# Performance work log

Measured on AMD Instinct MI355X. Metric: run time of the kernel, lower is better.

## Reference

```python
import jax, jax.numpy as jnp
from jax import lax
import numpy as np

SIGMA = 0.05  # perturbation std (module default)


def setup_inputs() -> dict:
    key = jax.random.key(0)
    k1, k2, k3 = jax.random.split(key, 3)
    return {
        "scores": jax.random.normal(k1, (8, 32, 32), dtype=jnp.float32),      # scorer output (b, h_score, w_score)
        "x_high": jax.random.normal(k2, (8, 3, 1024, 1024), dtype=jnp.float32),
        "noise": jax.random.normal(k3, (8, 500, 1024), dtype=jnp.float32),    # (b, num_samples, d)
        "k": 16,
        "patch_size": 64,
    }


def reference(scores, x_high, noise, k, patch_size):
    b, hs, ws = scores.shape
    _, c, H, W = x_high.shape
    d = hs * ws
    n = noise.shape[1]
    p = patch_size

    # --- min-max normalize scores (as in DPS.forward) ---
    s = scores.reshape(b, d)
    smin = s.min(axis=-1, keepdims=True)
    smax = s.max(axis=-1, keepdims=True)
    s = (s - smin) / (smax - smin + 1e-5)

    # --- PerturbedTopK forward: mean of one-hot top-k over noise samples ---
    perturbed = s[:, None, :] + noise * SIGMA            # (b, n, d)
    _, idx = lax.top_k(perturbed, k)                     # (b, n, k)
    idx = jnp.sort(idx, axis=-1)
    bi = jnp.arange(b)[:, None, None]
    ki = jnp.arange(k)[None, None, :]
    # scatter-count == one_hot(idx, d).mean(axis=1) without materializing (b,n,k,d)
    indicators = jnp.zeros((b, k, d), s.dtype).at[bi, ki, idx].add(1.0 / n)
    indicators = indicators.reshape(b, k, hs, ws)

    # --- pad high-res image exactly like DPS.__init__ ---
    sh, sw = H // hs, W // ws                            # scale_h, scale_w
    top = (p - sh) // 2
    left = (p - sw) // 2
    padded_h = sh * hs + p - 1
    padded_w = sw * ws + p - 1
    x_pad = jnp.pad(x_high, ((0, 0), (0, 0), (top, padded_h - top - H), (left, padded_w - left - W)))
    # only the first (hs-1)*sh + p rows/cols are ever sliced by the loop
    Eh = (hs - 1) * sh + p
    Ew = (ws - 1) * sw + p
    x_pad = x_pad[:, :, :Eh, :Ew]

    # --- weighted patch gather: sum_{i,j} ind[b,k,i,j] * x_pad[b,c, i*sh+u, j*sw+v]
    # expressed as a dilated-kernel cross-correlation, vmapped over batch.
    def per_b(xp, w):  # xp: (c, Eh, Ew), w: (k, hs, ws)
        out = lax.conv_general_dilated(
            xp[:, None],            # lhs (c, 1, Eh, Ew): channels act as batch
            w[:, None],             # rhs (k, 1, hs, ws)
            window_strides=(1, 1),
            padding="VALID",
            rhs_dilation=(sh, sw),
        )                           # (c, k, p, p)
        return out.transpose(1, 0, 2, 3)  # (k, c, p, p)

    patches = jax.vmap(per_b)(x_pad, indicators)  # (b, k, c, p, p)
    return patches
```

## Files before the change

### kernel.cpp

```cpp
#include <hip/hip_runtime.h>

constexpr int NB = 8;
constexpr int ND = 1024;
constexpr int NS = 500;
constexpr int NK = 16;
constexpr int NC = 3;
constexpr int NH = 1024;
constexpr int NW = 1024;
constexpr int SH = 32;
constexpr int SW = 32;
constexpr int NP = 64;
constexpr int PTOP = 16;
constexpr int PLEFT = 16;
constexpr float SIGMA = 0.05f;

__global__ void normalize_kernel(const float* __restrict__ scores,
                                 float* __restrict__ s_norm) {
    int b = blockIdx.x;
    int t = threadIdx.x;
    float v[4];
    float mn, mx;
#pragma unroll
    for (int q = 0; q < 4; q++) v[q] = scores[b * ND + t + 256 * q];
    mn = fminf(fminf(v[0], v[1]), fminf(v[2], v[3]));
    mx = fmaxf(fmaxf(v[0], v[1]), fmaxf(v[2], v[3]));
#pragma unroll
    for (int off = 1; off < 64; off <<= 1) {
        mn = fminf(mn, __shfl_xor(mn, off));
        mx = fmaxf(mx, __shfl_xor(mx, off));
    }
    __shared__ float smn[4], smx[4];
    int wave = t >> 6, lane = t & 63;
    if (lane == 0) { smn[wave] = mn; smx[wave] = mx; }
    __syncthreads();
    mn = fminf(fminf(smn[0], smn[1]), fminf(smn[2], smn[3]));
    mx = fmaxf(fmaxf(smx[0], smx[1]), fmaxf(smx[2], smx[3]));
    float den = mx - mn + 1e-5f;
#pragma unroll
    for (int q = 0; q < 4; q++)
        s_norm[b * ND + t + 256 * q] = (v[q] - mn) / den;
}

__global__ void topk_kernel(const float* __restrict__ s_norm,
                            const float* __restrict__ noise,
                            int* __restrict__ counts) {
    int t = threadIdx.x;
    int wave = t >> 6, lane = t & 63;
    int sid = blockIdx.x * 4 + wave;
    int b = sid / NS;

    const float* sp = s_norm + b * ND;
    const float* npp = noise + (size_t)sid * ND;

    float v[16];
#pragma unroll
    for (int q = 0; q < 16; q++) {
        int j = q * 64 + lane;
        v[q] = sp[j] + npp[j] * SIGMA;
    }

    int myj = 0x7fffffff;
    for (int it = 0; it < NK; it++) {
        float bv = v[0];
        int bq = 0;
#pragma unroll
        for (int q = 1; q < 16; q++)
            if (v[q] > bv) { bv = v[q]; bq = q; }
        int bj = bq * 64 + lane;
#pragma unroll
        for (int off = 1; off < 64; off <<= 1) {
            float ov = __shfl_xor(bv, off);
            int oj = __shfl_xor(bj, off);
            if (ov > bv || (ov == bv && oj < bj)) { bv = ov; bj = oj; }
        }
        if (lane == it) myj = bj;
        int wq = bj >> 6, wl = bj & 63;
#pragma unroll
        for (int q = 0; q < 16; q++)
            v[q] = (q == wq && lane == wl) ? -1e30f : v[q];
    }

    int rank = 0;
#pragma unroll
    for (int u = 0; u < NK; u++) {
        int other = __shfl(myj, u);
        rank += (other < myj) ? 1 : 0;
    }
    if (lane < NK)
        atomicAdd(&counts[(b * NK + rank) * ND + myj], 1);
}

__global__ void compact_kernel(const int* __restrict__ counts,
                               int* __restrict__ lists,
                               int* __restrict__ ncells) {
    int bk = blockIdx.x;
    int t = threadIdx.x;
    int lane = t & 63, wave = t >> 6;
    const int* cp = counts + bk * ND;

    int c4[4];
    int flags = 0, cnt = 0;
#pragma unroll
    for (int q = 0; q < 4; q++) {
        c4[q] = cp[t * 4 + q];
        if (c4[q] != 0) { flags |= 1 << q; cnt++; }
    }
    int incl = cnt;
#pragma unroll
    for (int off = 1; off < 64; off <<= 1) {
        int o = __shfl_up(incl, off);
        if (lane >= off) incl += o;
    }
    int excl = incl - cnt;
    __shared__ int wtot[4];
    if (lane == 63) wtot[wave] = incl;
    __syncthreads();
    int base = 0;
    for (int w = 0; w < wave; w++) base += wtot[w];
    int pos = base + excl;
    int* lp = lists + bk * NS;
#pragma unroll
    for (int q = 0; q < 4; q++) {
        if (flags & (1 << q)) {
            lp[pos++] = ((t * 4 + q) << 16) | c4[q];
        }
    }
    if (t == 0)
        ncells[bk] = wtot[0] + wtot[1] + wtot[2] + wtot[3];
}

__global__ void gather_kernel(const int* __restrict__ lists,
                              const int* __restrict__ ncells,
                              const float* __restrict__ x_high,
                              float* __restrict__ out) {
    int blk = blockIdx.x;
    int g = blk & 7;
    int c = (blk >> 3) % NC;
    int bk = blk / (NC * 8);
    int t = threadIdx.x;

    int n = ncells[bk];
    __shared__ int lst[NS];
    for (int i = t; i < n; i += 256) lst[i] = lists[bk * NS + i];
    __syncthreads();

    const float* xp = x_high + (size_t)((bk >> 4) * NC + c) * NH * NW;
    int x = t & 63;
    int yq = t >> 6;
    int y0 = g * 8 + yq;

    float a0 = 0.f, a1 = 0.f;
    const float invn = 1.0f / (float)NS;
    for (int e = 0; e < n; e++) {
        int pk = lst[e];
        int cell = pk >> 16;
        float w = (float)(pk & 0xffff) * invn;
        int i = cell >> 5;
        int j = cell & 31;
        int col = j * SW + x - PLEFT;
        bool colok = (unsigned)col < (unsigned)NW;
        int row0 = i * SH + y0 - PTOP;
        int row1 = row0 + 4;
        float v0 = (colok && (unsigned)row0 < (unsigned)NH)
                       ? xp[(size_t)row0 * NW + col] : 0.f;
        float v1 = (colok && (unsigned)row1 < (unsigned)NH)
                       ? xp[(size_t)row1 * NW + col] : 0.f;
        a0 += w * v0;
        a1 += w * v1;
    }

    float* op = out + (size_t)(bk * NC + c) * NP * NP;
    op[(g * 8 + yq) * NP + x] = a0;
    op[(g * 8 + yq + 4) * NP + x] = a1;
}

extern "C" void kernel_launch(void* const* d_in, const int* in_sizes, int n_in,
                              void* d_out, int out_size, void* d_ws, size_t ws_size,
                              hipStream_t stream) {
    const float* scores = (const float*)d_in[0];
    const float* x_high = (const float*)d_in[1];
    const float* noise  = (const float*)d_in[2];

    char* ws = (char*)d_ws;
    float* s_norm = (float*)ws;
    int* counts   = (int*)(ws + 32 * 1024);
    int* lists    = (int*)(ws + 32 * 1024 + 512 * 1024);
    int* ncells   = (int*)(ws + 32 * 1024 + 512 * 1024 + 256 * 1024);

    hipMemsetAsync(counts, 0, (size_t)NB * NK * ND * sizeof(int), stream);
    normalize_kernel<<<NB, 256, 0, stream>>>(scores, s_norm);
    topk_kernel<<<NB * NS / 4, 256, 0, stream>>>(s_norm, noise, counts);
    compact_kernel<<<NB * NK, 256, 0, stream>>>(counts, lists, ncells);
    gather_kernel<<<NB * NK * NC * 8, 256, 0, stream>>>(lists, ncells, x_high, (float*)d_out);
}
```

Measured before the change: 59.71 us.

## Gather over per-batch union of cells with 8 k-weights per load; fuse memset

Replaces the per-(b,k) compacted cell lists with one union list of nonzero cells per batch, storing 16 weights per cell. Each image pixel loaded in the gather is then reused for 8 output patches at once, cutting redundant global loads of x_high. The counts memset is folded into the normalize kernel to save a launch. The trade-off is that the union kernel runs on only 8 blocks with serial weight writes, and the gather grid shrinks to 768 blocks that each loop over the larger union list.

Result: slower. 88.72 us (+48.6%).

```diff
diff --git a/kernel.cpp b/kernel.cpp
--- a/kernel.cpp
+++ b/kernel.cpp
@@ -7,23 +7,28 @@
 constexpr int NC = 3;
 constexpr int NH = 1024;
 constexpr int NW = 1024;
-constexpr int SH = 32;
-constexpr int SW = 32;
 constexpr int NP = 64;
 constexpr int PTOP = 16;
 constexpr int PLEFT = 16;
 constexpr float SIGMA = 0.05f;
 
 __global__ void normalize_kernel(const float* __restrict__ scores,
-                                 float* __restrict__ s_norm) {
-    int b = blockIdx.x;
-    int t = threadIdx.x;
+                                 float* __restrict__ s_norm,
+                                 int* __restrict__ counts) {
+    int blk = blockIdx.x;
+    int t = threadIdx.x;
+
+    int4 z4 = make_int4(0, 0, 0, 0);
+    ((int4*)counts)[blk * 512 + t] = z4;
+    ((int4*)counts)[blk * 512 + 256 + t] = z4;
+
+    if (blk >= NB) return;
+    int b = blk;
     float v[4];
-    float mn, mx;
 #pragma unroll
     for (int q = 0; q < 4; q++) v[q] = scores[b * ND + t + 256 * q];
-    mn = fminf(fminf(v[0], v[1]), fminf(v[2], v[3]));
-    mx = fmaxf(fmaxf(v[0], v[1]), fmaxf(v[2], v[3]));
+    float mn = fminf(fminf(v[0], v[1]), fminf(v[2], v[3]));
+    float mx = fmaxf(fmaxf(v[0], v[1]), fmaxf(v[2], v[3]));
 #pragma unroll
     for (int off = 1; off < 64; off <<= 1) {
         mn = fminf(mn, __shfl_xor(mn, off));
@@ -90,21 +95,24 @@
         atomicAdd(&counts[(b * NK + rank) * ND + myj], 1);
 }
 
-__global__ void compact_kernel(const int* __restrict__ counts,
-                               int* __restrict__ lists,
-                               int* __restrict__ ncells) {
-    int bk = blockIdx.x;
+__global__ void union_kernel(const int* __restrict__ counts,
+                             int* __restrict__ ucell,
+                             float* __restrict__ uw,
+                             int* __restrict__ nunion) {
+    int b = blockIdx.x;
     int t = threadIdx.x;
     int lane = t & 63, wave = t >> 6;
-    const int* cp = counts + bk * ND;
-
-    int c4[4];
-    int flags = 0, cnt = 0;
-#pragma unroll
-    for (int q = 0; q < 4; q++) {
-        c4[q] = cp[t * 4 + q];
-        if (c4[q] != 0) { flags |= 1 << q; cnt++; }
-    }
+    const int* cp = counts + b * NK * ND;
+
+    unsigned nz = 0;
+    for (int kk = 0; kk < NK; kk++) {
+        int4 c4 = *(const int4*)(cp + kk * ND + t * 4);
+        if (c4.x) nz |= 1;
+        if (c4.y) nz |= 2;
+        if (c4.z) nz |= 4;
+        if (c4.w) nz |= 8;
+    }
+    int cnt = __popc(nz);
     int incl = cnt;
 #pragma unroll
     for (int off = 1; off < 64; off <<= 1) {
@@ -118,60 +126,86 @@
     int base = 0;
     for (int w = 0; w < wave; w++) base += wtot[w];
     int pos = base + excl;
-    int* lp = lists + bk * NS;
+
+    const float invn = 1.0f / (float)NS;
+    int* up = ucell + b * ND;
+    float* wp = uw + (size_t)b * ND * NK;
 #pragma unroll
     for (int q = 0; q < 4; q++) {
-        if (flags & (1 << q)) {
-            lp[pos++] = ((t * 4 + q) << 16) | c4[q];
-        }
-    }
-    if (t == 0)
-        ncells[bk] = wtot[0] + wtot[1] + wtot[2] + wtot[3];
-}
-
-__global__ void gather_kernel(const int* __restrict__ lists,
-                              const int* __restrict__ ncells,
+        if (nz & (1u << q)) {
+            int cell = t * 4 + q;
+            up[pos] = cell;
+            for (int kk = 0; kk < NK; kk++)
+                wp[(size_t)pos * NK + kk] = (float)cp[kk * ND + cell] * invn;
+            pos++;
+        }
+    }
+    if (t == 0) nunion[b] = wtot[0] + wtot[1] + wtot[2] + wtot[3];
+}
+
+constexpr int CH = 256;
+__global__ void gather_kernel(const int* __restrict__ ucell,
+                              const float* __restrict__ uw,
+                              const int* __restrict__ nunion,
                               const float* __restrict__ x_high,
                               float* __restrict__ out) {
     int blk = blockIdx.x;
-    int g = blk & 7;
-    int c = (blk >> 3) % NC;
-    int bk = blk / (NC * 8);
-    int t = threadIdx.x;
-
-    int n = ncells[bk];
-    __shared__ int lst[NS];
-    for (int i = t; i < n; i += 256) lst[i] = lists[bk * NS + i];
-    __syncthreads();
-
-    const float* xp = x_high + (size_t)((bk >> 4) * NC + c) * NH * NW;
+    int gg = blk & 15;
+    int kh = (blk >> 4) & 1;
+    int c = (blk >> 5) % NC;
+    int b = blk / (NC * 2 * 16);
+    int t = threadIdx.x;
     int x = t & 63;
     int yq = t >> 6;
-    int y0 = g * 8 + yq;
-
-    float a0 = 0.f, a1 = 0.f;
-    const float invn = 1.0f / (float)NS;
-    for (int e = 0; e < n; e++) {
-        int pk = lst[e];
-        int cell = pk >> 16;
-        float w = (float)(pk & 0xffff) * invn;
-        int i = cell >> 5;
-        int j = cell & 31;
-        int col = j * SW + x - PLEFT;
-        bool colok = (unsigned)col < (unsigned)NW;
-        int row0 = i * SH + y0 - PTOP;
-        int row1 = row0 + 4;
-        float v0 = (colok && (unsigned)row0 < (unsigned)NH)
-                       ? xp[(size_t)row0 * NW + col] : 0.f;
-        float v1 = (colok && (unsigned)row1 < (unsigned)NH)
-                       ? xp[(size_t)row1 * NW + col] : 0.f;
-        a0 += w * v0;
-        a1 += w * v1;
-    }
-
-    float* op = out + (size_t)(bk * NC + c) * NP * NP;
-    op[(g * 8 + yq) * NP + x] = a0;
-    op[(g * 8 + yq + 4) * NP + x] = a1;
+    int y = gg * 4 + yq;
+
+    int U = nunion[b];
+    __shared__ int lc[CH];
+    __shared__ float lw[CH][8];
+
+    const float* xp = x_high + (size_t)(b * NC + c) * NH * NW;
+    int xm = x - PLEFT;
+    int ym = y - PTOP;
+
+    float acc[8];
+#pragma unroll
+    for (int q = 0; q < 8; q++) acc[q] = 0.f;
+
+    for (int base = 0; base < U; base += CH) {
+        int m = min(CH, U - base);
+        __syncthreads();
+        if (t < m) {
+            lc[t] = ucell[b * ND + base + t];
+            const float4* wsrc =
+                (const float4*)(uw + ((size_t)b * ND + base + t) * NK + kh * 8);
+            *(float4*)&lw[t][0] = wsrc[0];
+            *(float4*)&lw[t][4] = wsrc[1];
+        }
+        __syncthreads();
+#pragma unroll 4
+        for (int e = 0; e < m; e++) {
+            int cell = lc[e];
+            int col = ((cell & 31) << 5) + xm;
+            int row = ((cell >> 5) << 5) + ym;
+            bool ok = ((unsigned)col < (unsigned)NW) & ((unsigned)row < (unsigned)NH);
+            int rc = min(max(row, 0), NH - 1);
+            int cc = min(max(col, 0), NW - 1);
+            float v = xp[(rc << 10) + cc];
+            v = ok ? v : 0.f;
+            float4 wa = *(const float4*)&lw[e][0];
+            float4 wb = *(const float4*)&lw[e][4];
+            acc[0] += wa.x * v; acc[1] += wa.y * v;
+            acc[2] += wa.z * v; acc[3] += wa.w * v;
+            acc[4] += wb.x * v; acc[5] += wb.y * v;
+            acc[6] += wb.z * v; acc[7] += wb.w * v;
+        }
+    }
+
+#pragma unroll
+    for (int q = 0; q < 8; q++) {
+        int o = ((b * NK + kh * 8 + q) * NC + c) * (NP * NP) + y * NP + x;
+        out[o] = acc[q];
+    }
 }
 
 extern "C" void kernel_launch(void* const* d_in, const int* in_sizes, int n_in,
@@ -184,12 +218,13 @@
     char* ws = (char*)d_ws;
     float* s_norm = (float*)ws;
     int* counts   = (int*)(ws + 32 * 1024);
-    int* lists    = (int*)(ws + 32 * 1024 + 512 * 1024);
-    int* ncells   = (int*)(ws + 32 * 1024 + 512 * 1024 + 256 * 1024);
-
-    hipMemsetAsync(counts, 0, (size_t)NB * NK * ND * sizeof(int), stream);
-    normalize_kernel<<<NB, 256, 0, stream>>>(scores, s_norm);
+    int* ucell    = (int*)(ws + 544 * 1024);
+    float* uw     = (float*)(ws + 576 * 1024);
+    int* nunion   = (int*)(ws + 1088 * 1024);
+
+    normalize_kernel<<<64, 256, 0, stream>>>(scores, s_norm, counts);
     topk_kernel<<<NB * NS / 4, 256, 0, stream>>>(s_norm, noise, counts);
-    compact_kernel<<<NB * NK, 256, 0, stream>>>(counts, lists, ncells);
-    gather_kernel<<<NB * NK * NC * 8, 256, 0, stream>>>(lists, ncells, x_high, (float*)d_out);
-}
+    union_kernel<<<NB, 256, 0, stream>>>(counts, ucell, uw, nunion);
+    gather_kernel<<<NB * NC * 2 * 16, 256, 0, stream>>>(ucell, uw, nunion, x_high,
+                                                        (float*)d_out);
+}
```
